# Performance work log

Measured on AMD Instinct MI355X. Metric: run time of the kernel, lower is better.

The kernel has to match this reference:

```python
import jax, jax.numpy as jnp
import numpy as np

B, P, K, H = 8, 4096, 20, 128  # graphs, points per graph, kNN, hidden_channels


def _linear_init(key, fin, fout):
    s = 1.0 / np.sqrt(fin)
    kw, kb = jax.random.split(key)
    W = jax.random.uniform(kw, (fin, fout), jnp.float32, -s, s)
    b = jax.random.uniform(kb, (fout,), jnp.float32, -s, s)
    return W, b


def setup_inputs() -> dict:
    key = jax.random.key(0)
    ks = jax.random.split(key, 6)
    x = jax.random.normal(ks[0], (B, P, 3), jnp.float32)
    W1, b1 = _linear_init(ks[1], 2 * 3, H)
    W2, b2 = _linear_init(ks[2], 2 * H, H)
    W3, b3 = _linear_init(ks[3], 2 * H, H)
    W4, b4 = _linear_init(ks[4], H, H)
    W5, b5 = _linear_init(ks[5], H, 3)
    return dict(x=x, W1=W1, b1=b1, W2=W2, b2=b2, W3=W3, b3=b3,
                W4=W4, b4=b4, W5=W5, b5=b5)


def _dynamic_edge_conv(x, W, b):
    # x: [B, P, D]. Recompute kNN graph in feature space, EdgeConv with max aggr.
    sq = jnp.sum(x * x, axis=-1)                                   # [B, P]
    d2 = sq[:, :, None] + sq[:, None, :] - 2.0 * jnp.einsum('bid,bjd->bij', x, x)
    eye = jnp.eye(x.shape[1], dtype=bool)                          # exclude self-loops
    d2 = jnp.where(eye[None], jnp.inf, d2)
    _, idx = jax.lax.top_k(-d2, K)                                 # [B, P, K]
    xj = jax.vmap(lambda xb, ib: xb[ib])(x, idx)                   # [B, P, K, D] gather
    xi = jnp.broadcast_to(x[:, :, None, :], xj.shape)
    e = jnp.concatenate([xi, xj - xi], axis=-1)                    # [B, P, K, 2D]
    h = jax.nn.relu(e @ W + b)                                     # edge MLP
    return jnp.max(h, axis=2)                                      # max aggregation -> [B, P, H]


def reference(x, W1, b1, W2, b2, W3, b3, W4, b4, W5, b5):
    h = jax.nn.relu(_dynamic_edge_conv(x, W1, b1))
    h = jax.nn.relu(_dynamic_edge_conv(h, W2, b2))
    h = jax.nn.relu(_dynamic_edge_conv(h, W3, b3))
    g = jnp.mean(h, axis=1)                                        # global_mean_pool -> [B, H]
    g = jax.nn.relu(g @ W4 + b4)
    # dropout is identity in eval mode
    return g @ W5 + b5                                             # [B, 3]
```

## Files before the change

### kernel.cpp

```cpp
#include <hip/hip_runtime.h>
#include <hip/hip_bf16.h>


static constexpr int B_ = 8, P_ = 4096, K_ = 20, H_ = 128;
static constexpr float FINF = 3.0e38f;
static constexpr int CAPH = 192;

typedef __attribute__((ext_vector_type(8))) short short8;
typedef __attribute__((ext_vector_type(16))) float floatx16;

__device__ __forceinline__ float dist3(float x0, float x1, float x2,
                                       const float4& v) {
  return fmaf(-2.f, fmaf(x0, v.x, fmaf(x1, v.y, x2 * v.z)), v.w);
}

__device__ __forceinline__ void cvt_split(float v, ushort& h, ushort& l) {
  __hip_bfloat16 hb = __float2bfloat16(v);
  float hf = __bfloat162float(hb);
  __hip_bfloat16 lb = __float2bfloat16(v - hf);
  h = *(ushort*)&hb;
  l = *(ushort*)&lb;
}

__global__ __launch_bounds__(256) void feat3p_kernel(
    const float* __restrict__ X, const float* __restrict__ W,
    const float* __restrict__ bias, float* __restrict__ c_out,
    float* __restrict__ u_out, float4* __restrict__ pt4) {
  const int h = threadIdx.x & (H_ - 1);
  const int pg = threadIdx.x >> 7;
  const int bb = blockIdx.x & 7;
  const int pb = blockIdx.x >> 3;
  const int pbase = bb * P_ + pb * 8;
  const int p0 = pbase + pg * 4;
  if (threadIdx.x < 8) {
    const float* row = X + (size_t)(pbase + threadIdx.x) * 3;
    float4 v;
    v.x = row[0]; v.y = row[1]; v.z = row[2];
    v.w = fmaf(v.x, v.x, fmaf(v.y, v.y, v.z * v.z));
    pt4[pbase + threadIdx.x] = v;
  }
  float a0 = 0, a1 = 0, a2 = 0, a3 = 0, u0 = 0, u1 = 0, u2 = 0, u3 = 0;
  const float* xp = X + (size_t)p0 * 3;
#pragma unroll
  for (int d = 0; d < 3; ++d) {
    float wt = W[d * H_ + h];
    float wb = W[(3 + d) * H_ + h];
    float x0 = xp[d], x1 = xp[3 + d], x2 = xp[6 + d], x3 = xp[9 + d];
    a0 = fmaf(x0, wt, a0); u0 = fmaf(x0, wb, u0);
    a1 = fmaf(x1, wt, a1); u1 = fmaf(x1, wb, u1);
    a2 = fmaf(x2, wt, a2); u2 = fmaf(x2, wb, u2);
    a3 = fmaf(x3, wt, a3); u3 = fmaf(x3, wb, u3);
  }
  float bv = bias[h];
  c_out[(size_t)(p0 + 0) * H_ + h] = a0 - u0 + bv;
  c_out[(size_t)(p0 + 1) * H_ + h] = a1 - u1 + bv;
  c_out[(size_t)(p0 + 2) * H_ + h] = a2 - u2 + bv;
  c_out[(size_t)(p0 + 3) * H_ + h] = a3 - u3 + bv;
  u_out[(size_t)(p0 + 0) * H_ + h] = u0;
  u_out[(size_t)(p0 + 1) * H_ + h] = u1;
  u_out[(size_t)(p0 + 2) * H_ + h] = u2;
  u_out[(size_t)(p0 + 3) * H_ + h] = u3;
}

__global__ __launch_bounds__(256) void wprep2_kernel(
    const float* __restrict__ W2, const float* __restrict__ W3,
    ushort* __restrict__ Vfh2, ushort* __restrict__ Vfl2,
    ushort* __restrict__ Vfh3, ushort* __restrict__ Vfl3) {
  const int which = blockIdx.x >> 4;
  const float* W = which ? W3 : W2;
  ushort* Vfh = which ? Vfh3 : Vfh2;
  ushort* Vfl = which ? Vfl3 : Vfl2;
  int tid = (blockIdx.x & 15) * 256 + threadIdx.x;
  int t = tid >> 9;
  int s = (tid >> 6) & 7;
  int lane = tid & 63;
  int col = t * 32 + (lane & 31);
  int kb = s * 16 + ((lane >> 5) << 3);
  ushort h[8], l[8];
#pragma unroll
  for (int e = 0; e < 8; ++e) {
    int k = kb + e;
    float v;
    if (col < 128) v = W[k * H_ + col] - W[(128 + k) * H_ + col];
    else v = W[(128 + k) * H_ + col - 128];
    cvt_split(v, h[e], l[e]);
  }
  size_t off = (size_t)((t * 8 + s) * 64 + lane) * 8;
  *(short8*)(Vfh + off) = *(short8*)h;
  *(short8*)(Vfl + off) = *(short8*)l;
}

__device__ __forceinline__ void stage_async(const ushort* __restrict__ Xhi,
                                            const ushort* __restrict__ Xlo,
                                            size_t tile, char* buf, int w,
                                            int lane) {
  const char* gh = (const char*)(Xhi + tile);
  const char* gl = (const char*)(Xlo + tile);
  const int lo16 = lane * 16;
#pragma unroll
  for (int it = 0; it < 4; ++it) {
    const int off = (w * 4 + it) * 1024;
    __builtin_amdgcn_global_load_lds(
        (const __attribute__((address_space(1))) void*)(gh + off + lo16),
        (__attribute__((address_space(3))) void*)(buf + off), 16, 0, 0);
    __builtin_amdgcn_global_load_lds(
        (const __attribute__((address_space(1))) void*)(gl + off + lo16),
        (__attribute__((address_space(3))) void*)(buf + 16384 + off), 16, 0, 0);
  }
}

__device__ __forceinline__ void stage_async32(const ushort* __restrict__ Xhi,
                                              const ushort* __restrict__ Xlo,
                                              size_t tile, char* buf, int w,
                                              int lane) {
  const char* gh = (const char*)(Xhi + tile);
  const char* gl = (const char*)(Xlo + tile);
  const int lo16 = lane * 16;
#pragma unroll
  for (int it = 0; it < 4; ++it) {
    const int off = (w * 4 + it) * 1024;
    __builtin_amdgcn_global_load_lds(
        (const __attribute__((address_space(1))) void*)(gh + off + lo16),
        (__attribute__((address_space(3))) void*)(buf + off), 16, 0, 0);
    __builtin_amdgcn_global_load_lds(
        (const __attribute__((address_space(1))) void*)(gl + off + lo16),
        (__attribute__((address_space(3))) void*)(buf + 8192 + off), 16, 0, 0);
  }
}

__device__ __forceinline__ void load_afrag_sw(const ushort* __restrict__ X,
                                              size_t gb, int row, int lane,
                                              short8* a) {
  const ushort* base = X + (gb + row) * (size_t)H_;
  const int x = row & 15;
  const int kh = lane >> 5;
#pragma unroll
  for (int s = 0; s < 8; ++s) {
    a[s] = *(const short8*)(base + (((s * 2 + kh) ^ x) << 3));
  }
}

__device__ __forceinline__ floatx16 gram32(const char* lds, const short8* ahi,
                                           const short8* alo, int jh,
                                           int lane) {
  floatx16 a0, a1, a2;
#pragma unroll
  for (int i = 0; i < 16; ++i) { a0[i] = 0.f; a1[i] = 0.f; a2[i] = 0.f; }
  const int base = (jh * 32 + (lane & 31)) * 256;
  const int kh = lane >> 5;
  const int x = lane & 15;
#pragma unroll
  for (int s = 0; s < 8; ++s) {
    const int off = base + (((s * 2 + kh) ^ x) << 4);
    short8 bh = *(const short8*)(lds + off);
    short8 bl = *(const short8*)(lds + 16384 + off);
    a0 = __builtin_amdgcn_mfma_f32_32x32x16_bf16(ahi[s], bh, a0, 0, 0, 0);
    a1 = __builtin_amdgcn_mfma_f32_32x32x16_bf16(ahi[s], bl, a1, 0, 0, 0);
    a2 = __builtin_amdgcn_mfma_f32_32x32x16_bf16(alo[s], bh, a2, 0, 0, 0);
  }
  floatx16 acc;
#pragma unroll
  for (int i = 0; i < 16; ++i) acc[i] = (a0[i] + a1[i]) + a2[i];
  return acc;
}

__device__ __forceinline__ floatx16 gram32t(const char* lds, const short8* ahi,
                                            const short8* alo, int lane) {
  floatx16 a0, a1, a2;
#pragma unroll
  for (int i = 0; i < 16; ++i) { a0[i] = 0.f; a1[i] = 0.f; a2[i] = 0.f; }
  const int base = (lane & 31) * 256;
  const int kh = lane >> 5;
  const int x = lane & 15;
#pragma unroll
  for (int s = 0; s < 8; ++s) {
    const int off = base + (((s * 2 + kh) ^ x) << 4);
    short8 bh = *(const short8*)(lds + off);
    short8 bl = *(const short8*)(lds + 8192 + off);
    a0 = __builtin_amdgcn_mfma_f32_32x32x16_bf16(ahi[s], bh, a0, 0, 0, 0);
    a1 = __builtin_amdgcn_mfma_f32_32x32x16_bf16(ahi[s], bl, a1, 0, 0, 0);
    a2 = __builtin_amdgcn_mfma_f32_32x32x16_bf16(alo[s], bh, a2, 0, 0, 0);
  }
  floatx16 acc;
#pragma unroll
  for (int i = 0; i < 16; ++i) acc[i] = (a0[i] + a1[i]) + a2[i];
  return acc;
}

__device__ __forceinline__ float kth20_of32(float* v) {
  float m = 0.f;
  for (int sel = 0; sel < K_; ++sel) {
    m = v[0];
#pragma unroll
    for (int t = 1; t < 32; ++t) m = fminf(m, v[t]);
    bool done = false;
#pragma unroll
    for (int t = 0; t < 32; ++t) {
      if (!done && v[t] == m) { v[t] = FINF; done = true; }
    }
  }
  return m;
}

__global__ __launch_bounds__(256) void featpart_kernel(
    const ushort* __restrict__ Xhi, const ushort* __restrict__ Xlo,
    const ushort* __restrict__ Vfh, const ushort* __restrict__ Vfl,
    const float* __restrict__ bias, float* __restrict__ c_out,
    float* __restrict__ u_out, const float* __restrict__ sqn,
    float* __restrict__ tau) {
  __shared__ char buf[32768];
  __shared__ float ldist[64 * 65];

  const int tid = threadIdx.x;
  const int lane = tid & 63;
  const int w = tid >> 6;
  const int rh = w >> 1, jh = w & 1;
  const int b = blockIdx.x & 7;
  const int i0 = (blockIdx.x >> 3) * 64;
  const size_t gb = (size_t)b * P_;

  short8 ahi[8], alo[8];
  const int arow = i0 + rh * 32 + (lane & 31);
  load_afrag_sw(Xhi, gb, arow, lane, ahi);
  load_afrag_sw(Xlo, gb, arow, lane, alo);

  const int rl = 4 * (lane >> 5);
#pragma unroll
  for (int tt = 0; tt < 4; ++tt) {
    const int t = jh * 4 + tt;
    floatx16 a0, a1, a2;
#pragma unroll
    for (int i = 0; i < 16; ++i) { a0[i] = 0.f; a1[i] = 0.f; a2[i] = 0.f; }
#pragma unroll
    for (int s = 0; s < 8; ++s) {
      const size_t off = (size_t)((t * 8 + s) * 64 + lane) * 8;
      short8 bh = *(const short8*)(Vfh + off);
      short8 bl = *(const short8*)(Vfl + off);
      a0 = __builtin_amdgcn_mfma_f32_32x32x16_bf16(ahi[s], bh, a0, 0, 0, 0);
      a1 = __builtin_amdgcn_mfma_f32_32x32x16_bf16(ahi[s], bl, a1, 0, 0, 0);
      a2 = __builtin_amdgcn_mfma_f32_32x32x16_bf16(alo[s], bh, a2, 0, 0, 0);
    }
    const int col = t * 32 + (lane & 31);
    if (jh == 0) {
      float bv = bias[col];
#pragma unroll
      for (int g = 0; g < 16; ++g) {
        int row = i0 + rh * 32 + rl + (g & 3) + 8 * (g >> 2);
        c_out[(gb + row) * (size_t)H_ + col] = ((a0[g] + a1[g]) + a2[g]) + bv;
      }
    } else {
#pragma unroll
      for (int g = 0; g < 16; ++g) {
        int row = i0 + rh * 32 + rl + (g & 3) + 8 * (g >> 2);
        u_out[(gb + row) * (size_t)H_ + col - 128] = (a0[g] + a1[g]) + a2[g];
      }
    }
  }

  const int rowb = rh * 32 + rl;
  const int jcol = jh * 32 + (lane & 31);
  const int srow = tid >> 2;
  const int sr = tid & 3;
  const int gi = i0 + srow;
  float bd[8];

#pragma unroll
  for (int ch = 0; ch < 8; ++ch) {
    const int tb = ch * 64;
    stage_async(Xhi, Xlo, (gb + tb) * (size_t)H_, buf, w, lane);
    float sqv = sqn[gb + tb + jcol];
    __syncthreads();
    floatx16 acc = gram32(buf, ahi, alo, jh, lane);
#pragma unroll
    for (int g = 0; g < 16; ++g) {
      ldist[(rowb + (g & 3) + 8 * (g >> 2)) * 65 + jcol] =
          fmaf(-2.f, acc[g], sqv);
    }
    __syncthreads();
    const float* drow = ldist + srow * 65 + sr * 16;
    float m = FINF;
#pragma unroll
    for (int jj = 0; jj < 16; ++jj) {
      float s = drow[jj];
      int jg = tb + sr * 16 + jj;
      m = (jg == gi) ? m : fminf(m, s);
    }
    bd[ch] = m;
  }
  __syncthreads();
#pragma unroll
  for (int k = 0; k < 8; ++k) ldist[srow * 65 + sr * 8 + k] = bd[k];
  __syncthreads();
  if (sr == 0) {
    float v[32];
#pragma unroll
    for (int t = 0; t < 32; ++t) v[t] = ldist[srow * 65 + t];
    tau[gb + gi] = kth20_of32(v);
  }
}

__global__ __launch_bounds__(128) void knn_compact_kernel(
    const ushort* __restrict__ Xhi, const ushort* __restrict__ Xlo,
    const float* __restrict__ sqn, const float* __restrict__ tau,
    float2* __restrict__ cand, int* __restrict__ cnt) {
  __shared__ char buf[2][16384];

  const int tid = threadIdx.x;
  const int lane = tid & 63;
  const int w = tid >> 6;
  const int b = blockIdx.x & 7;
  const int rest = blockIdx.x >> 3;
  const int half = rest & 1;
  const int i0 = (rest >> 1) * 64;
  const size_t gb = (size_t)b * P_;

  short8 ahi[8], alo[8];
  const int arow = i0 + w * 32 + (lane & 31);
  load_afrag_sw(Xhi, gb, arow, lane, ahi);
  load_afrag_sw(Xlo, gb, arow, lane, alo);

  const int rowb = i0 + w * 32 + 4 * (lane >> 5);
  float taur[16];
  int cur[16];
#pragma unroll
  for (int g = 0; g < 16; ++g) {
    taur[g] = tau[gb + rowb + (g & 3) + 8 * (g >> 2)];
    cur[g] = 0;
  }
  float2* candrow = cand + (gb + rowb) * (size_t)(2 * CAPH) + half * CAPH;
  const unsigned lmask = (1u << (lane & 31)) - 1u;
  const int jbase = half * 2048;

  stage_async32(Xhi, Xlo, (gb + jbase) * (size_t)H_, buf[0], w, lane);
  float sqv_next = sqn[gb + jbase + (lane & 31)];

  for (int c = 0; c < 64; ++c) {
    const int tb = jbase + c * 32;
    __syncthreads();
    float sqv = sqv_next;
    if (c < 63) {
      stage_async32(Xhi, Xlo, (gb + tb + 32) * (size_t)H_, buf[(c + 1) & 1], w,
                    lane);
      sqv_next = sqn[gb + tb + 32 + (lane & 31)];
    }
    floatx16 acc = gram32t(buf[c & 1], ahi, alo, lane);
    const int jg = tb + (lane & 31);
#pragma unroll
    for (int g = 0; g < 16; ++g) {
      float d = fmaf(-2.f, acc[g], sqv);
      bool pred = (d <= taur[g]);
      unsigned long long mk = __ballot(pred);
      if (mk) {
        unsigned seg = (lane >= 32) ? (unsigned)(mk >> 32) : (unsigned)mk;
        int idx = cur[g] + __popc(seg & lmask);
        if (pred && idx < CAPH) {
          float2 e;
          e.x = d;
          e.y = __int_as_float(jg);
          candrow[(size_t)((g & 3) + 8 * (g >> 2)) * (2 * CAPH) + idx] = e;
        }
        cur[g] += __popc(seg);
      }
    }
  }
  if ((lane & 31) == 0) {
#pragma unroll
    for (int g = 0; g < 16; ++g) {
      int row = rowb + (g & 3) + 8 * (g >> 2);
      cnt[(gb + row) * 2 + half] = cur[g] < CAPH ? cur[g] : CAPH;
    }
  }
}

__global__ __launch_bounds__(256) void knn3_full_kernel(
    const float4* __restrict__ pt4, float2* __restrict__ cand,
    int* __restrict__ cnt) {
  __shared__ float lv[64 * 33];
  __shared__ float ltau[64];
  const int tid = threadIdx.x;
  const int b = blockIdx.x & 7;
  const int rest = blockIdx.x >> 3;
  const int half = rest & 1;
  const int i0 = (rest >> 1) * 64;
  const size_t gb = (size_t)b * P_;

  {
    const int row_local = tid >> 2;
    const int r = tid & 3;
    const int gi = i0 + row_local;
    float4 pi = pt4[gb + gi];
    const float4* pg = pt4 + gb + r * 256;
    float bd[8];
#pragma unroll
    for (int s = 0; s < 8; ++s) {
      float m = FINF;
#pragma unroll 4
      for (int jj = 0; jj < 32; ++jj) {
        int jl = s * 32 + jj;
        float4 v = pg[jl];
        float d = dist3(pi.x, pi.y, pi.z, v);
        int jg = r * 256 + jl;
        m = (jg == gi) ? m : fminf(m, d);
      }
      bd[s] = m;
    }
#pragma unroll
    for (int k = 0; k < 8; ++k) lv[row_local * 33 + r * 8 + k] = bd[k];
    __syncthreads();
    if (r == 0) {
      float v[32];
#pragma unroll
      for (int t = 0; t < 32; ++t) v[t] = lv[row_local * 33 + t];
      ltau[row_local] = kth20_of32(v);
    }
  }
  __syncthreads();

  const int lane = tid & 63;
  const int w = tid >> 6;
  const int r0 = i0 + w * 16;
  float xr0[16], xr1[16], xr2[16], taur[16];
  int cur[16];
#pragma unroll
  for (int r = 0; r < 16; ++r) {
    float4 p = pt4[gb + r0 + r];
    xr0[r] = p.x; xr1[r] = p.y; xr2[r] = p.z;
    taur[r] = ltau[w * 16 + r];
    cur[r] = 0;
  }
  const float4* pg = pt4 + gb + half * 2048;
  for (int ch = 0; ch < 32; ++ch) {
    float4 v = pg[ch * 64 + lane];
    int jg = half * 2048 + ch * 64 + lane;
#pragma unroll
    for (int r = 0; r < 16; ++r) {
      float d = dist3(xr0[r], xr1[r], xr2[r], v);
      bool pred = (d <= taur[r]);
      unsigned long long mk = __ballot(pred);
      if (mk) {
        int n = __popcll(mk);
        int pre = __popcll(mk & ((1ull << lane) - 1ull));
        int idx = cur[r] + pre;
        if (pred && idx < CAPH) {
          float2 e;
          e.x = d;
          e.y = __int_as_float(jg);
          cand[(gb + r0 + r) * (size_t)(2 * CAPH) + half * CAPH + idx] = e;
        }
        cur[r] += n;
      }
    }
  }
  if (lane == 0) {
#pragma unroll
    for (int r = 0; r < 16; ++r)
      cnt[(gb + r0 + r) * 2 + half] = cur[r] < CAPH ? cur[r] : CAPH;
  }
}

__global__ __launch_bounds__(256) void selsplit_kernel(
    const float2* __restrict__ cand, const int* __restrict__ cnt,
    const float* __restrict__ c, const float* __restrict__ u,
    float* __restrict__ out, ushort* __restrict__ hi,
    ushort* __restrict__ lo, float* __restrict__ sqn) {
  __shared__ int ljs[4][24];
  __shared__ float aggv[4][128];
  const int w = threadIdx.x >> 6;
  const int lane = threadIdx.x & 63;
  const int b = blockIdx.x & 7;
  const int rowbase = b * P_ + (blockIdx.x >> 3) * 4;
  const int row = rowbase + w;
  const int c0 = cnt[row * 2], c1 = cnt[row * 2 + 1];
  const int ctot = c0 + c1;
  float d[6];
  int j[6];
#pragma unroll
  for (int s = 0; s < 6; ++s) {
    int m = s * 64 + lane;
    bool valid = m < ctot;
    int addr = (m < c0) ? m : (CAPH + m - c0);
    if (!valid) addr = 0;
    float2 e = cand[(size_t)row * (2 * CAPH) + addr];
    d[s] = valid ? e.x : FINF;
    j[s] = __float_as_int(e.y);
  }
  for (int round = 0; round < K_ + 1; ++round) {
    float bm = d[0];
    int bs = 0;
#pragma unroll
    for (int s = 1; s < 6; ++s) {
      if (d[s] < bm) { bm = d[s]; bs = s; }
    }
    int id = (lane << 3) | bs;
#pragma unroll
    for (int off = 1; off < 64; off <<= 1) {
      float od = __shfl_xor(bm, off);
      int oid = __shfl_xor(id, off);
      if (od < bm || (od == bm && oid < id)) { bm = od; id = oid; }
    }
    int owner = id >> 3, os = id & 7;
    if (lane == owner) {
      int jv = 0;
#pragma unroll
      for (int s = 0; s < 6; ++s) {
        if (s == os) { jv = j[s]; d[s] = FINF; }
      }
      ljs[w][round] = jv;
    }
  }
  const float2* c2p = (const float2*)(c + (size_t)row * H_);
  float2 ci = c2p[lane];
  float mx = 0.f, my = 0.f;
#pragma unroll 4
  for (int k = 1; k <= K_; ++k) {
    int jj = ljs[w][k];
    float2 uv = *(const float2*)(u + ((size_t)(b << 12) + jj) * H_ + lane * 2);
    mx = fmaxf(mx, ci.x + uv.x);
    my = fmaxf(my, ci.y + uv.y);
  }
  if (out != nullptr) {
    float2 o;
    o.x = mx; o.y = my;
    *(float2*)(out + (size_t)row * H_ + lane * 2) = o;
  }
  if (hi != nullptr) {
    aggv[w][lane * 2] = mx;
    aggv[w][lane * 2 + 1] = my;
    __syncthreads();
    const int tid = threadIdx.x;
    if (tid < 64) {
      const int r = tid >> 4, m = tid & 15;
      const int rrow = rowbase + r;
      float vv[8];
      float ss = 0.f;
      ushort hh[8], ll[8];
#pragma unroll
      for (int e = 0; e < 8; ++e) {
        vv[e] = aggv[r][m * 8 + e];
        ss = fmaf(vv[e], vv[e], ss);
        cvt_split(vv[e], hh[e], ll[e]);
      }
      size_t dst = ((size_t)rrow << 7) + ((size_t)(m ^ (rrow & 15)) << 3);
      *(short8*)(hi + dst) = *(short8*)hh;
      *(short8*)(lo + dst) = *(short8*)ll;
#pragma unroll
      for (int off = 1; off < 16; off <<= 1) ss += __shfl_xor(ss, off);
      if (m == 0) sqn[rrow] = ss;
    }
  }
}

__global__ __launch_bounds__(128) void pool_kernel(const float* __restrict__ hf,
                                                   float* __restrict__ psum) {
  constexpr int CHUNK = 64;
  int blk = blockIdx.x;
  int b = blk >> 6;
  int chunk = blk & 63;
  int h = threadIdx.x;
  int base = (b << 12) + chunk * CHUNK;
  float acc = 0.f;
#pragma unroll 4
  for (int p = 0; p < CHUNK; ++p) acc += hf[(size_t)(base + p) * H_ + h];
  psum[blk * H_ + h] = acc;
}

__global__ __launch_bounds__(128) void head_kernel(
    const float* __restrict__ psum, const float* __restrict__ W4,
    const float* __restrict__ b4, const float* __restrict__ W5,
    const float* __restrict__ b5, float* __restrict__ out) {
  int b = blockIdx.x, h = threadIdx.x;
  __shared__ float g[H_];
  __shared__ float t[H_];
  float s = 0.f;
#pragma unroll 4
  for (int ch = 0; ch < 64; ++ch) s += psum[(b * 64 + ch) * H_ + h];
  g[h] = s * (1.0f / P_);
  __syncthreads();
  float acc = b4[h];
#pragma unroll 4
  for (int d = 0; d < H_; ++d) acc = fmaf(g[d], W4[d * H_ + h], acc);
  t[h] = fmaxf(acc, 0.f);
  __syncthreads();
  if (h < 3) {
    float o = b5[h];
#pragma unroll 4
    for (int d = 0; d < H_; ++d) o = fmaf(t[d], W5[d * 3 + h], o);
    out[b * 3 + h] = o;
  }
}

extern "C" void kernel_launch(void* const* d_in, const int* in_sizes, int n_in,
                              void* d_out, int out_size, void* d_ws,
                              size_t ws_size, hipStream_t stream) {
  const float* x  = (const float*)d_in[0];
  const float* W1 = (const float*)d_in[1];
  const float* b1 = (const float*)d_in[2];
  const float* W2 = (const float*)d_in[3];
  const float* b2 = (const float*)d_in[4];
  const float* W3 = (const float*)d_in[5];
  const float* b3 = (const float*)d_in[6];
  const float* W4 = (const float*)d_in[7];
  const float* b4 = (const float*)d_in[8];
  const float* W5 = (const float*)d_in[9];
  const float* b5 = (const float*)d_in[10];
  float* out = (float*)d_out;

  char* ws = (char*)d_ws;
  const size_t NF = (size_t)B_ * P_ * H_;
  const size_t NP_ = (size_t)B_ * P_;
  float*  bufA = (float*)ws;  ws += NF * 4;
  float*  bufB = (float*)ws;  ws += NF * 4;
  float*  bufU = (float*)ws;  ws += NF * 4;
  ushort* xhi  = (ushort*)ws; ws += NF * 2;
  ushort* xlo  = (ushort*)ws; ws += NF * 2;
  float*  sqn  = (float*)ws;  ws += NP_ * 4;
  float*  psum = (float*)ws;  ws += (size_t)B_ * 64 * H_ * 4;
  float*  tau  = (float*)ws;  ws += NP_ * 4;
  int*    cnt  = (int*)ws;    ws += NP_ * 2 * 4;
  float4* pt4  = (float4*)ws; ws += NP_ * 16;
  ushort* vfh2 = (ushort*)ws; ws += 32768 * 2;
  ushort* vfl2 = (ushort*)ws; ws += 32768 * 2;
  ushort* vfh3 = (ushort*)ws; ws += 32768 * 2;
  ushort* vfl3 = (ushort*)ws; ws += 32768 * 2;
  float2* cand = (float2*)ws; ws += NP_ * (size_t)(2 * CAPH) * 8;

  const int NP = B_ * P_;
  dim3 blk256(256), blk128(128);

  wprep2_kernel<<<32, blk256, 0, stream>>>(W2, W3, vfh2, vfl2, vfh3, vfl3);

  feat3p_kernel<<<NP / 8, blk256, 0, stream>>>(x, W1, b1, bufA, bufU, pt4);
  knn3_full_kernel<<<B_ * 64 * 2, blk256, 0, stream>>>(pt4, cand, cnt);
  selsplit_kernel<<<NP / 4, blk256, 0, stream>>>(cand, cnt, bufA, bufU,
                                                 nullptr, xhi, xlo, sqn);

  featpart_kernel<<<B_ * 64, blk256, 0, stream>>>(xhi, xlo, vfh2, vfl2, b2,
                                                  bufB, bufU, sqn, tau);
  knn_compact_kernel<<<B_ * 64 * 2, blk128, 0, stream>>>(xhi, xlo, sqn, tau,
                                                         cand, cnt);
  selsplit_kernel<<<NP / 4, blk256, 0, stream>>>(cand, cnt, bufB, bufU,
                                                 nullptr, xhi, xlo, sqn);

  featpart_kernel<<<B_ * 64, blk256, 0, stream>>>(xhi, xlo, vfh3, vfl3, b3,
                                                  bufB, bufU, sqn, tau);
  knn_compact_kernel<<<B_ * 64 * 2, blk128, 0, stream>>>(xhi, xlo, sqn, tau,
                                                         cand, cnt);
  selsplit_kernel<<<NP / 4, blk256, 0, stream>>>(cand, cnt, bufB, bufU,
                                                 bufA, nullptr, nullptr,
                                                 nullptr);

  pool_kernel<<<B_ * 64, blk128, 0, stream>>>(bufA, psum);
  head_kernel<<<B_, blk128, 0, stream>>>(psum, W4, b4, W5, b5, out);
}
```

Baseline: 1.068 ms.

## Parallelize kth-20 threshold selection across 4 lanes and merge knn3 halves

Replaces the serial single-thread 20th-smallest selection over 32 block minima with a 4-lane cooperative version. Each lane holds 8 values and repeatedly removes the max via xor shuffles, dropping 12 of 32 so the remaining max is the 20th smallest. This removes an LDS round trip and two barriers in featpart and knn3_full. knn3_full now processes all 4096 columns in one block instead of two halves, which halves the grid and avoids recomputing tau twice. It adds a software prefetch of the next column chunk and writes a single candidate segment of capacity 2*CAPH, at the cost of fewer blocks and longer serial loops.

```diff
diff --git a/kernel.cpp b/kernel.cpp
--- a/kernel.cpp
+++ b/kernel.cpp
@@ -20,6 +20,32 @@
   __hip_bfloat16 lb = __float2bfloat16(v - hf);
   h = *(ushort*)&hb;
   l = *(ushort*)&lb;
+}
+
+__device__ __forceinline__ float kth20_par4(float* v, int lane) {
+  const int sub = lane & 3;
+  for (int r = 0; r < 12; ++r) {
+    float lm = v[0];
+    int la = 0;
+#pragma unroll
+    for (int t = 1; t < 8; ++t) {
+      if (v[t] > lm) { lm = v[t]; la = t; }
+    }
+    int gid = sub * 8 + la;
+#pragma unroll
+    for (int off = 1; off < 4; off <<= 1) {
+      float om = __shfl_xor(lm, off);
+      int oid = __shfl_xor(gid, off);
+      if (om > lm || (om == lm && oid > gid)) { lm = om; gid = oid; }
+    }
+    if ((gid >> 3) == sub) v[gid & 7] = -FINF;
+  }
+  float lm = v[0];
+#pragma unroll
+  for (int t = 1; t < 8; ++t) lm = fmaxf(lm, v[t]);
+#pragma unroll
+  for (int off = 1; off < 4; off <<= 1) lm = fmaxf(lm, __shfl_xor(lm, off));
+  return lm;
 }
 
 __global__ __launch_bounds__(256) void feat3p_kernel(
@@ -187,21 +213,6 @@
   return acc;
 }
 
-__device__ __forceinline__ float kth20_of32(float* v) {
-  float m = 0.f;
-  for (int sel = 0; sel < K_; ++sel) {
-    m = v[0];
-#pragma unroll
-    for (int t = 1; t < 32; ++t) m = fminf(m, v[t]);
-    bool done = false;
-#pragma unroll
-    for (int t = 0; t < 32; ++t) {
-      if (!done && v[t] == m) { v[t] = FINF; done = true; }
-    }
-  }
-  return m;
-}
-
 __global__ __launch_bounds__(256) void featpart_kernel(
     const ushort* __restrict__ Xhi, const ushort* __restrict__ Xlo,
     const ushort* __restrict__ Vfh, const ushort* __restrict__ Vfl,
@@ -287,16 +298,8 @@
     }
     bd[ch] = m;
   }
-  __syncthreads();
-#pragma unroll
-  for (int k = 0; k < 8; ++k) ldist[srow * 65 + sr * 8 + k] = bd[k];
-  __syncthreads();
-  if (sr == 0) {
-    float v[32];
-#pragma unroll
-    for (int t = 0; t < 32; ++t) v[t] = ldist[srow * 65 + t];
-    tau[gb + gi] = kth20_of32(v);
-  }
+  float t20 = kth20_par4(bd, lane);
+  if (sr == 0) tau[gb + gi] = t20;
 }
 
 __global__ __launch_bounds__(128) void knn_compact_kernel(
@@ -375,13 +378,10 @@
 __global__ __launch_bounds__(256) void knn3_full_kernel(
     const float4* __restrict__ pt4, float2* __restrict__ cand,
     int* __restrict__ cnt) {
-  __shared__ float lv[64 * 33];
   __shared__ float ltau[64];
   const int tid = threadIdx.x;
   const int b = blockIdx.x & 7;
-  const int rest = blockIdx.x >> 3;
-  const int half = rest & 1;
-  const int i0 = (rest >> 1) * 64;
+  const int i0 = (blockIdx.x >> 3) * 64;
   const size_t gb = (size_t)b * P_;
 
   {
@@ -404,15 +404,8 @@
       }
       bd[s] = m;
     }
-#pragma unroll
-    for (int k = 0; k < 8; ++k) lv[row_local * 33 + r * 8 + k] = bd[k];
-    __syncthreads();
-    if (r == 0) {
-      float v[32];
-#pragma unroll
-      for (int t = 0; t < 32; ++t) v[t] = lv[row_local * 33 + t];
-      ltau[row_local] = kth20_of32(v);
-    }
+    float t20 = kth20_par4(bd, tid & 63);
+    if (r == 0) ltau[row_local] = t20;
   }
   __syncthreads();
 
@@ -428,10 +421,12 @@
     taur[r] = ltau[w * 16 + r];
     cur[r] = 0;
   }
-  const float4* pg = pt4 + gb + half * 2048;
-  for (int ch = 0; ch < 32; ++ch) {
-    float4 v = pg[ch * 64 + lane];
-    int jg = half * 2048 + ch * 64 + lane;
+  const float4* pg = pt4 + gb;
+  float4 v = pg[lane];
+  for (int ch = 0; ch < 64; ++ch) {
+    float4 vn;
+    if (ch < 63) vn = pg[(ch + 1) * 64 + lane];
+    const int jg = ch * 64 + lane;
 #pragma unroll
     for (int r = 0; r < 16; ++r) {
       float d = dist3(xr0[r], xr1[r], xr2[r], v);
@@ -441,20 +436,23 @@
         int n = __popcll(mk);
         int pre = __popcll(mk & ((1ull << lane) - 1ull));
         int idx = cur[r] + pre;
-        if (pred && idx < CAPH) {
+        if (pred && idx < 2 * CAPH) {
           float2 e;
           e.x = d;
           e.y = __int_as_float(jg);
-          cand[(gb + r0 + r) * (size_t)(2 * CAPH) + half * CAPH + idx] = e;
+          cand[(gb + r0 + r) * (size_t)(2 * CAPH) + idx] = e;
         }
         cur[r] += n;
       }
     }
+    v = vn;
   }
   if (lane == 0) {
 #pragma unroll
-    for (int r = 0; r < 16; ++r)
-      cnt[(gb + r0 + r) * 2 + half] = cur[r] < CAPH ? cur[r] : CAPH;
+    for (int r = 0; r < 16; ++r) {
+      cnt[(gb + r0 + r) * 2] = cur[r] < 2 * CAPH ? cur[r] : 2 * CAPH;
+      cnt[(gb + r0 + r) * 2 + 1] = 0;
+    }
   }
 }
 
@@ -630,7 +628,7 @@
   wprep2_kernel<<<32, blk256, 0, stream>>>(W2, W3, vfh2, vfl2, vfh3, vfl3);
 
   feat3p_kernel<<<NP / 8, blk256, 0, stream>>>(x, W1, b1, bufA, bufU, pt4);
-  knn3_full_kernel<<<B_ * 64 * 2, blk256, 0, stream>>>(pt4, cand, cnt);
+  knn3_full_kernel<<<B_ * 64, blk256, 0, stream>>>(pt4, cand, cnt);
   selsplit_kernel<<<NP / 4, blk256, 0, stream>>>(cand, cnt, bufA, bufU,
                                                  nullptr, xhi, xlo, sqn);
 
```

Result: faster. 919.7 us (-13.9%).
